# Kernel optimization log

Measured on AMD Instinct MI355X. Metric: run time of the kernel, lower is better.

## Reference

```python
import math
import jax, jax.numpy as jnp
import numpy as np

NUM_HEADS = 32

def _alibi_slopes(n: int) -> jnp.ndarray:
    cp2 = 2 ** int(math.floor(math.log2(n)))
    base = 2.0 ** (-(2.0 ** (-(math.log2(cp2) - 3))))
    slopes = base ** np.arange(1, cp2 + 1, dtype=np.float64)
    if cp2 != n:
        extra_base = 2.0 ** (-(2.0 ** (-(math.log2(2 * cp2) - 3))))
        rem = min(cp2, n - cp2)
        slopes = np.concatenate([slopes, extra_base ** np.arange(1, 1 + 2 * rem, 2, dtype=np.float64)])
    return jnp.asarray(slopes, dtype=jnp.float32)


def setup_inputs() -> dict:
    key = jax.random.key(0)
    k1, k2, k3 = jax.random.split(key, 3)
    B, S, E, H, D = 2, 2048, 4096, NUM_HEADS, 128
    hidden_states = jax.random.normal(k1, (B, S, E), dtype=jnp.float32)
    # torch Linear y = x @ W^T; we store transposed weights [in, out]
    w_qkv = jax.random.normal(k2, (E, H * D + 2 * D), dtype=jnp.float32) * 0.02
    w_c = jax.random.normal(k3, (E, E), dtype=jnp.float32) * 0.02
    return {"hidden_states": hidden_states, "w_qkv": w_qkv, "w_c": w_c}


def reference(hidden_states, w_qkv, w_c):
    B, S, E = hidden_states.shape
    H = NUM_HEADS
    D = E // H
    scaling = D ** -0.5

    qkv = hidden_states @ w_qkv                      # [B,S,H*D+2D]
    q = qkv[..., : H * D].reshape(B, S, H, D)        # [B,S,H,D]
    k = qkv[..., H * D: H * D + D]                   # [B,S,D] single KV head (MQA)
    v = qkv[..., H * D + D:]                         # [B,S,D]

    pos = jnp.arange(S)
    slopes = _alibi_slopes(H)                        # [H]
    # ALiBi: slope * (k_pos - q_pos), <= 0 in the causal region
    bias = slopes[:, None, None] * (pos[None, None, :] - pos[None, :, None]).astype(jnp.float32)  # [H,S,S]

    scores = jnp.einsum('bqhd,bkd->bhqk', q, k) * scaling + bias[None]  # [B,H,S,S]
    causal = pos[:, None] >= pos[None, :]            # [S,S]
    scores = jnp.where(causal[None, None], scores, jnp.finfo(scores.dtype).min)
    probs = jax.nn.softmax(scores, axis=-1)
    attn = jnp.einsum('bhqk,bkd->bqhd', probs, v).reshape(B, S, E)
    return attn @ w_c
```

## Files before the change

kernel.cpp:

```cpp
#include <hip/hip_runtime.h>
#include <hip/hip_bf16.h>

typedef unsigned short u16;
typedef unsigned int u32;
typedef __attribute__((ext_vector_type(8))) short s16x8;
typedef __attribute__((ext_vector_type(4))) float f32x4;

#define MFMA_BF16(a, b, c) __builtin_amdgcn_mfma_f32_16x16x32_bf16(a, b, c, 0, 0, 0)

__device__ __forceinline__ u16 f2bf(float f) {
  union { float f; u32 u; } c; c.f = f;
  return (u16)((c.u + 0x7FFFu + ((c.u >> 16) & 1u)) >> 16);
}

__device__ __forceinline__ u32 pkbf(float a, float b) {
  float2 t; t.x = a; t.y = b;
  __hip_bfloat162 h = __float22bfloat162_rn(t);
  union { __hip_bfloat162 h; u32 u; } c; c.h = h; return c.u;
}

__device__ __forceinline__ void gll16(const void* g, void* l) {
  __builtin_amdgcn_global_load_lds((const __attribute__((address_space(1))) void*)g,
                                   (__attribute__((address_space(3))) void*)l, 16, 0, 0);
}

__device__ __forceinline__ f32x4 f4zero() { f32x4 z = {0.f, 0.f, 0.f, 0.f}; return z; }

__global__ void cvt_bf16_kernel(const float4* __restrict__ in, u16* __restrict__ out, int n4) {
  int i = blockIdx.x * 256 + threadIdx.x;
  if (i >= n4) return;
  float4 v = in[i];
  uint2 w;
  w.x = (u32)f2bf(v.x) | ((u32)f2bf(v.y) << 16);
  w.y = (u32)f2bf(v.z) | ((u32)f2bf(v.w) << 16);
  *reinterpret_cast<uint2*>(out + (size_t)i * 4) = w;
}

__global__ void transpose_cvt_kernel(const float* __restrict__ in, u16* __restrict__ out,
                                     int R, int C) {
  __shared__ float tile[32][33];
  int tx = threadIdx.x, ty = threadIdx.y;
  int r0 = blockIdx.y * 32, c0 = blockIdx.x * 32;
#pragma unroll
  for (int i = 0; i < 32; i += 8)
    tile[ty + i][tx] = in[(size_t)(r0 + ty + i) * C + c0 + tx];
  __syncthreads();
#pragma unroll
  for (int i = 0; i < 32; i += 8)
    out[(size_t)(c0 + ty + i) * R + r0 + tx] = f2bf(tile[tx][ty + i]);
}


#define BARRIER __builtin_amdgcn_s_barrier()
#define SCHEDB __builtin_amdgcn_sched_barrier(0)
#define PRIO1 __builtin_amdgcn_s_setprio(1)
#define PRIO0 __builtin_amdgcn_s_setprio(0)
#define VM0 asm volatile("s_waitcnt vmcnt(0)" ::: "memory")

#define RDAB(PR) do { _Pragma("unroll")                                                  \
  for (int mi2 = 0; mi2 < 4; ++mi2)                                                      \
    a[mi2] = *(const s16x8*)(smem + (PR)*8192 + aOff + mi2*1024);                        \
  _Pragma("unroll")                                                                      \
  for (int ni2 = 0; ni2 < 4; ++ni2)                                                      \
    b[ni2] = *(const s16x8*)(smem + 16384 + (PR)*16384 + bOff + ni2*1024);               \
} while (0)

#define MFMA16 do { _Pragma("unroll")                                                    \
  for (int mi2 = 0; mi2 < 4; ++mi2) { _Pragma("unroll")                                  \
    for (int ni2 = 0; ni2 < 4; ++ni2)                                                    \
      acc[mi2][ni2] = MFMA_BF16(a[mi2], b[ni2], acc[mi2][ni2]);                          \
  } } while (0)

#define STAGE3(PW, kn) do {                                                              \
  gll16(srcA + (kn), smem + (PW)*8192 + tt*16);                                          \
  gll16(srcB0 + (kn), smem + 16384 + (PW)*16384 + tt*16);                                \
  gll16(srcB1 + (kn), smem + 16384 + (PW)*16384 + 8192 + tt*16);                         \
} while (0)

#define TILE(PR, PW, T, LAST) do {                                                      \
  s16x8 a[4], b[4];                                                                      \
  RDAB(PR);                                                                              \
  if (!(LAST)) { STAGE3(PW, ((T) + 1) * 32); }                                           \
  SCHEDB;                                                                                \
  PRIO1; MFMA16; PRIO0;                                                                  \
  SCHEDB;                                                                                \
  VM0;                                                                                   \
  BARRIER;                                                                               \
} while (0)

template<int EPI>
__global__ __launch_bounds__(512, 4)
void gemm128_kernel(const u16* __restrict__ A, const u16* __restrict__ Bt,
                    float* __restrict__ Cf, u16* __restrict__ Cq,
                    u16* __restrict__ Ck, u16* __restrict__ Cvt,
                    int N, int K) {
  __shared__ __align__(16) char smem[49152];
  const int tt = threadIdx.x;
  const int w = tt >> 6, l = tt & 63;
  const int li = l & 15, g = l >> 4;
  const int wm = w >> 2, wn = w & 3;

  const int gx = gridDim.x;
  const int nwg = gx * gridDim.y;
  int id = blockIdx.y * gx + blockIdx.x;
  id = (id & 7) * (nwg >> 3) + (id >> 3);
  const int bn = id % gx, bm = id / gx;

  f32x4 acc[4][4];
#pragma unroll
  for (int i = 0; i < 4; ++i)
#pragma unroll
    for (int j = 0; j < 4; ++j) acc[i][j] = f4zero();

  const int gl = (tt & 3) ^ ((tt >> 2) & 3);
  const u16* srcA = A + (size_t)(bm * 128 + (tt >> 2)) * K + gl * 8;
  const u16* srcB0 = Bt + (size_t)(bn * 256 + (tt >> 2)) * K + gl * 8;
  const u16* srcB1 = srcB0 + (size_t)128 * K;

  const int gsw = (g ^ (li & 3)) * 16;
  const int aOff = (wm * 64 + li) * 64 + gsw;
  const int bOff = (wn * 64 + li) * 64 + gsw;

  STAGE3(0, 0);
  VM0;
  BARRIER;

  for (int t2 = 0; t2 < 126; t2 += 2) {
    TILE(0, 1, t2, 0);
    TILE(1, 0, t2 + 1, 0);
  }
  TILE(0, 1, 126, 0);
  TILE(1, 0, 127, 1);

#pragma unroll
  for (int mi = 0; mi < 4; ++mi) {
#pragma unroll
    for (int ni = 0; ni < 4; ++ni) {
      const int row0 = bm * 128 + wm * 64 + mi * 16 + g * 4;
      const int col = bn * 256 + wn * 64 + ni * 16 + li;
#pragma unroll
      for (int r = 0; r < 4; ++r) {
        const int m = row0 + r;
        const float v = acc[mi][ni][r];
        if (EPI == 0) {
          Cf[(size_t)m * N + col] = v;
        } else {
          const int bb2 = m >> 11, s = m & 2047;
          const int kt = s >> 5;
          const size_t tb = (size_t)(bb2 * 64 + kt);
          if (col < 4096) {
            Cq[(size_t)m * 4096 + col] = f2bf(v);
          } else if (col < 4224) {
            const int d = col - 4096, kr = s & 31;
            const int mk = kr >> 4, lii = kr & 15;
            const int kk = d >> 5, gg = (d >> 3) & 3, e = d & 7;
            Ck[(tb * 8 + mk * 4 + kk) * 512 + (gg * 16 + lii) * 8 + e] = f2bf(v);
          } else {
            const int d = col - 4224, kp = s & 31;
            const int mf = d >> 4, lii = d & 15;
            const int gg = kp >> 3, e = kp & 7;
            Cvt[(tb * 8 + mf) * 512 + (gg * 16 + lii) * 8 + e] = f2bf(v);
          }
        }
      }
    }
  }
}


__device__ __forceinline__ void load_ktile(s16x8 (&dst)[8], const u16* kf, size_t tb, int l) {
#pragma unroll
  for (int f = 0; f < 8; ++f)
    dst[f] = *(const s16x8*)&kf[(tb * 8 + f) * 512 + l * 8];
}

template<bool DIAG>
__device__ __forceinline__ void attn_tile(
    int kt, const u16* kf, const u16* vf, size_t bb64, int l, int li, int g,
    s16x8 (&use)[8], s16x8 (&fill)[8], bool do_fill,
    const s16x8 (&bq)[2][4], f32x4 (&acc)[8][2],
    float (&m_)[2], float (&lp)[2], float (&bias)[2],
    float c1, const float (&cjr)[8], float bstep, u16 (*Pw)[40]) {
  const size_t tb = bb64 + kt;
  s16x8 vr[8];
#pragma unroll
  for (int f = 0; f < 8; ++f)
    vr[f] = *(const s16x8*)&vf[(tb * 8 + f) * 512 + l * 8];
  if (do_fill) load_ktile(fill, kf, tb - 1, l);

  f32x4 sc[2][2];
  sc[0][0] = f4zero(); sc[0][1] = f4zero(); sc[1][0] = f4zero(); sc[1][1] = f4zero();
#pragma unroll
  for (int kk = 0; kk < 4; ++kk)
#pragma unroll
    for (int mk = 0; mk < 2; ++mk) {
      sc[mk][0] = MFMA_BF16(use[mk * 4 + kk], bq[0][kk], sc[mk][0]);
      sc[mk][1] = MFMA_BF16(use[mk * 4 + kk], bq[1][kk], sc[mk][1]);
    }

#pragma unroll
  for (int nq = 0; nq < 2; ++nq) {
    float sv[8];
    float pm = -3e38f;
    if (DIAG) {
#pragma unroll
      for (int mk = 0; mk < 2; ++mk)
#pragma unroll
        for (int r = 0; r < 4; ++r) {
          const int kd = mk * 16 + g * 4 + r - (nq * 16 + li);
          float s = fmaf(sc[mk][nq][r], c1, bias[nq] + cjr[mk * 4 + r]);
          s = (kd <= 0) ? s : -1e30f;
          sv[mk * 4 + r] = s;
          pm = fmaxf(pm, s);
        }
      pm = fmaxf(pm, __shfl_xor(pm, 16));
      pm = fmaxf(pm, __shfl_xor(pm, 32));
      m_[nq] = pm;
    } else {
#pragma unroll
      for (int mk = 0; mk < 2; ++mk)
#pragma unroll
        for (int r = 0; r < 4; ++r) {
          float s = fmaf(sc[mk][nq][r], c1, bias[nq] + cjr[mk * 4 + r]);
          sv[mk * 4 + r] = s;
          pm = fmaxf(pm, s);
        }
      if (__any(pm > m_[nq])) {
        pm = fmaxf(pm, __shfl_xor(pm, 16));
        pm = fmaxf(pm, __shfl_xor(pm, 32));
        const float nm = fmaxf(m_[nq], pm);
        const float scale = exp2f(m_[nq] - nm);
#pragma unroll
        for (int mf = 0; mf < 8; ++mf) acc[mf][nq] *= scale;
        lp[nq] *= scale;
        m_[nq] = nm;
      }
    }
    const float mref = m_[nq];
    float e[8];
#pragma unroll
    for (int j = 0; j < 8; ++j) e[j] = exp2f(sv[j] - mref);
    lp[nq] += ((e[0] + e[1]) + (e[2] + e[3])) + ((e[4] + e[5]) + (e[6] + e[7]));
#pragma unroll
    for (int mk = 0; mk < 2; ++mk) {
      uint2 wv;
      wv.x = pkbf(e[mk * 4 + 0], e[mk * 4 + 1]);
      wv.y = pkbf(e[mk * 4 + 2], e[mk * 4 + 3]);
      *reinterpret_cast<uint2*>(&Pw[nq * 16 + li][mk * 16 + g * 4]) = wv;
    }
    bias[nq] -= bstep;
  }

  s16x8 pb0 = *(const s16x8*)&Pw[li][g * 8];
  s16x8 pb1 = *(const s16x8*)&Pw[16 + li][g * 8];
#pragma unroll
  for (int mf = 0; mf < 8; ++mf) {
    acc[mf][0] = MFMA_BF16(vr[mf], pb0, acc[mf][0]);
    acc[mf][1] = MFMA_BF16(vr[mf], pb1, acc[mf][1]);
  }
}

__device__ __forceinline__ void attn_qtile(
    int qt, int h, int b, const u16* qbuf, const u16* kf, const u16* vf,
    u16* obuf, int l, int li, int g, float c1, float sl2, u16 (*Pw)[40]) {
  const int S = 2048;
  const int q0 = qt * 32;
  const size_t bb64 = (size_t)b * 64;

  s16x8 bq[2][4];
#pragma unroll
  for (int nq = 0; nq < 2; ++nq)
#pragma unroll
    for (int kk = 0; kk < 4; ++kk)
      bq[nq][kk] = *(const s16x8*)&qbuf[(size_t)(b * S + q0 + nq * 16 + li) * 4096
                                        + h * 128 + kk * 32 + g * 8];

  f32x4 acc[8][2];
#pragma unroll
  for (int mf = 0; mf < 8; ++mf) { acc[mf][0] = f4zero(); acc[mf][1] = f4zero(); }
  float m_[2] = {-3e38f, -3e38f};
  float lp[2] = {0.f, 0.f};

  float cjr[8];
#pragma unroll
  for (int j = 0; j < 8; ++j) cjr[j] = sl2 * (float)((j >> 2) * 16 + (j & 3));
  float bias[2];
#pragma unroll
  for (int nq = 0; nq < 2; ++nq)
    bias[nq] = sl2 * (float)(g * 4 - nq * 16 - li);
  const float bstep = sl2 * 32.f;

  s16x8 kA[8], kB[8];
  load_ktile(kA, kf, bb64 + qt, l);
  attn_tile<true>(qt, kf, vf, bb64, l, li, g, kA, kB, qt >= 1,
                  bq, acc, m_, lp, bias, c1, cjr, bstep, Pw);
  int kt = qt - 1;
  while (kt >= 1) {
    attn_tile<false>(kt, kf, vf, bb64, l, li, g, kB, kA, true,
                     bq, acc, m_, lp, bias, c1, cjr, bstep, Pw);
    attn_tile<false>(kt - 1, kf, vf, bb64, l, li, g, kA, kB, kt >= 2,
                     bq, acc, m_, lp, bias, c1, cjr, bstep, Pw);
    kt -= 2;
  }
  if (kt == 0)
    attn_tile<false>(0, kf, vf, bb64, l, li, g, kB, kA, false,
                     bq, acc, m_, lp, bias, c1, cjr, bstep, Pw);

#pragma unroll
  for (int nq = 0; nq < 2; ++nq) {
    float ls = lp[nq];
    ls += __shfl_xor(ls, 16);
    ls += __shfl_xor(ls, 32);
    const float inv = 1.f / ls;
    const size_t rowbase = (size_t)(b * S + q0 + nq * 16 + li) * 4096 + h * 128;
#pragma unroll
    for (int mf = 0; mf < 8; ++mf) {
      f32x4 v = acc[mf][nq];
      uint2 wv;
      wv.x = pkbf(v[0] * inv, v[1] * inv);
      wv.y = pkbf(v[2] * inv, v[3] * inv);
      *reinterpret_cast<uint2*>(&obuf[rowbase + mf * 16 + g * 4]) = wv;
    }
  }
}

__global__ __launch_bounds__(64, 2)
void attn_kernel(const u16* __restrict__ qbuf, const u16* __restrict__ kf,
                 const u16* __restrict__ vf, u16* __restrict__ obuf) {
  const int p = blockIdx.x, h = blockIdx.y, b = blockIdx.z;
  const int l = threadIdx.x, li = l & 15, g = l >> 4;
  const float L2E = 1.4426950408889634f;
  const float slope = exp2f(-0.25f * (float)(h + 1));
  const float c1 = 0.08838834764831845f * L2E;
  const float sl2 = slope * L2E;
  __shared__ __align__(16) u16 P[32][40];
  attn_qtile(63 - p, h, b, qbuf, kf, vf, obuf, l, li, g, c1, sl2, P);
  attn_qtile(p, h, b, qbuf, kf, vf, obuf, l, li, g, c1, sl2, P);
}

extern "C" void kernel_launch(void* const* d_in, const int* in_sizes, int n_in,
                              void* d_out, int out_size, void* d_ws, size_t ws_size,
                              hipStream_t stream) {
  (void)in_sizes; (void)n_in; (void)out_size; (void)ws_size;
  const float* hidden = (const float*)d_in[0];
  const float* w_qkv = (const float*)d_in[1];
  const float* w_c = (const float*)d_in[2];
  float* out = (float*)d_out;
  char* ws = (char*)d_ws;

  u16* hid_bf = (u16*)(ws + 0);
  u16* wT     = (u16*)(ws + 33554432);
  u16* qbuf   = (u16*)(ws + 69206016);
  u16* kbuf   = (u16*)(ws + 102760448);
  u16* vtbuf  = (u16*)(ws + 103809024);

  cvt_bf16_kernel<<<16384, 256, 0, stream>>>((const float4*)hidden, hid_bf, 4194304);
  transpose_cvt_kernel<<<dim3(136, 128), dim3(32, 8), 0, stream>>>(w_qkv, wT, 4096, 4352);
  gemm128_kernel<1><<<dim3(17, 32), 512, 0, stream>>>(hid_bf, wT, nullptr, qbuf, kbuf, vtbuf,
                                                      4352, 4096);
  attn_kernel<<<dim3(32, 32, 2), 64, 0, stream>>>(qbuf, kbuf, vtbuf, hid_bf);
  transpose_cvt_kernel<<<dim3(128, 128), dim3(32, 8), 0, stream>>>(w_c, wT, 4096, 4096);
  gemm128_kernel<0><<<dim3(16, 32), 512, 0, stream>>>(hid_bf, wT, out, nullptr, nullptr, nullptr,
                                                      4096, 4096);
}
```

Baseline: 510.1 us.

## Triple-buffer GEMM LDS staging with two tiles in flight and new swizzle

Moves the 128x256 GEMM main loop from double to triple buffering in LDS (48KB to 72KB). Global-to-LDS loads are issued two K-tiles ahead and the wait relaxes to vmcnt(3), so a tile's loads can still be in flight while the current one is computed. It also changes the staging address mapping and read swizzle to an 8-slot XOR pattern over two rows per 128-byte line, aimed at cutting LDS bank conflicts. The larger shared allocation may reduce the number of workgroups resident per CU.

```diff
diff --git a/kernel.cpp b/kernel.cpp
--- a/kernel.cpp
+++ b/kernel.cpp
@@ -55,14 +55,19 @@
 #define SCHEDB __builtin_amdgcn_sched_barrier(0)
 #define PRIO1 __builtin_amdgcn_s_setprio(1)
 #define PRIO0 __builtin_amdgcn_s_setprio(0)
+#define VM3 asm volatile("s_waitcnt vmcnt(3)" ::: "memory")
 #define VM0 asm volatile("s_waitcnt vmcnt(0)" ::: "memory")
-
-#define RDAB(PR) do { _Pragma("unroll")                                                  \
+#define NOPW do {} while (0)
+
+#define PAB(P) ((P) * 8192)
+#define PBB(P) (24576 + (P) * 16384)
+
+#define RDAB(P) do { _Pragma("unroll")                                                   \
   for (int mi2 = 0; mi2 < 4; ++mi2)                                                      \
-    a[mi2] = *(const s16x8*)(smem + (PR)*8192 + aOff + mi2*1024);                        \
+    a[mi2] = *(const s16x8*)(smem + PAB(P) + aOff + mi2*1024);                           \
   _Pragma("unroll")                                                                      \
   for (int ni2 = 0; ni2 < 4; ++ni2)                                                      \
-    b[ni2] = *(const s16x8*)(smem + 16384 + (PR)*16384 + bOff + ni2*1024);               \
+    b[ni2] = *(const s16x8*)(smem + PBB(P) + bOff + ni2*1024);                           \
 } while (0)
 
 #define MFMA16 do { _Pragma("unroll")                                                    \
@@ -71,20 +76,30 @@
       acc[mi2][ni2] = MFMA_BF16(a[mi2], b[ni2], acc[mi2][ni2]);                          \
   } } while (0)
 
-#define STAGE3(PW, kn) do {                                                              \
-  gll16(srcA + (kn), smem + (PW)*8192 + tt*16);                                          \
-  gll16(srcB0 + (kn), smem + 16384 + (PW)*16384 + tt*16);                                \
-  gll16(srcB1 + (kn), smem + 16384 + (PW)*16384 + 8192 + tt*16);                         \
+#define STAGE3(P, kn) do {                                                               \
+  gll16(srcA + (kn), smem + PAB(P) + tt*16);                                             \
+  gll16(srcB0 + (kn), smem + PBB(P) + tt*16);                                            \
+  gll16(srcB1 + (kn), smem + PBB(P) + 8192 + tt*16);                                     \
 } while (0)
 
-#define TILE(PR, PW, T, LAST) do {                                                      \
+#define TILE_S(PR, PS, T) do {                                                           \
   s16x8 a[4], b[4];                                                                      \
   RDAB(PR);                                                                              \
-  if (!(LAST)) { STAGE3(PW, ((T) + 1) * 32); }                                           \
+  STAGE3(PS, ((T) + 2) * 32);                                                            \
   SCHEDB;                                                                                \
   PRIO1; MFMA16; PRIO0;                                                                  \
   SCHEDB;                                                                                \
-  VM0;                                                                                   \
+  VM3;                                                                                   \
+  BARRIER;                                                                               \
+} while (0)
+
+#define TILE_T(PR, WAIT) do {                                                            \
+  s16x8 a[4], b[4];                                                                      \
+  RDAB(PR);                                                                              \
+  SCHEDB;                                                                                \
+  PRIO1; MFMA16; PRIO0;                                                                  \
+  SCHEDB;                                                                                \
+  WAIT;                                                                                  \
   BARRIER;                                                                               \
 } while (0)
 
@@ -94,7 +109,7 @@
                     float* __restrict__ Cf, u16* __restrict__ Cq,
                     u16* __restrict__ Ck, u16* __restrict__ Cvt,
                     int N, int K) {
-  __shared__ __align__(16) char smem[49152];
+  __shared__ __align__(16) char smem[73728];
   const int tt = threadIdx.x;
   const int w = tt >> 6, l = tt & 63;
   const int li = l & 15, g = l >> 4;
@@ -112,25 +127,29 @@
 #pragma unroll
     for (int j = 0; j < 4; ++j) acc[i][j] = f4zero();
 
-  const int gl = (tt & 3) ^ ((tt >> 2) & 3);
-  const u16* srcA = A + (size_t)(bm * 128 + (tt >> 2)) * K + gl * 8;
-  const u16* srcB0 = Bt + (size_t)(bn * 256 + (tt >> 2)) * K + gl * 8;
+  const int sg = (tt & 7) ^ ((tt >> 3) & 7);
+  const int ar = 2 * (tt >> 3) + (sg >> 2);
+  const int aq = sg & 3;
+  const u16* srcA = A + (size_t)(bm * 128 + ar) * K + aq * 8;
+  const u16* srcB0 = Bt + (size_t)(bn * 256 + ar) * K + aq * 8;
   const u16* srcB1 = srcB0 + (size_t)128 * K;
 
-  const int gsw = (g ^ (li & 3)) * 16;
-  const int aOff = (wm * 64 + li) * 64 + gsw;
-  const int bOff = (wn * 64 + li) * 64 + gsw;
+  const int slot = (((li & 1) * 4 + g) ^ ((li >> 1) & 7)) * 16;
+  const int aOff = wm * 4096 + (li >> 1) * 128 + slot;
+  const int bOff = wn * 4096 + (li >> 1) * 128 + slot;
 
   STAGE3(0, 0);
-  VM0;
+  STAGE3(1, 32);
+  VM3;
   BARRIER;
 
-  for (int t2 = 0; t2 < 126; t2 += 2) {
-    TILE(0, 1, t2, 0);
-    TILE(1, 0, t2 + 1, 0);
-  }
-  TILE(0, 1, 126, 0);
-  TILE(1, 0, 127, 1);
+  for (int t3 = 0; t3 < 126; t3 += 3) {
+    TILE_S(0, 2, t3);
+    TILE_S(1, 0, t3 + 1);
+    TILE_S(2, 1, t3 + 2);
+  }
+  TILE_T(0, VM0);
+  TILE_T(1, NOPW);
 
 #pragma unroll
   for (int mi = 0; mi < 4; ++mi) {
```

New measurement: 486.3 us. 4.7% less time.
